# Kernel optimization log

Measured on AMD Instinct MI355X. Metric: run time of the kernel, lower is better.

Reference implementation:

```python
import jax, jax.numpy as jnp
import numpy as np

N_NODES = 100000
N_EDGES = 500000
D_IN = 128
D_HID = 256
D_OUT = 1


def mish(x):
    # x * tanh(softplus(x))
    return x * jnp.tanh(jax.nn.softplus(x))


def setup_inputs() -> dict:
    key = jax.random.key(0)
    k1, k2, k3, k4, k5, k6 = jax.random.split(key, 6)
    z = jax.random.normal(k1, (N_NODES, D_IN), dtype=jnp.float32)
    edge = jax.random.randint(k2, (2, N_EDGES), 0, N_NODES, dtype=jnp.int64)
    # PyTorch Linear default init: U(-1/sqrt(fan_in), 1/sqrt(fan_in))
    s1 = 1.0 / np.sqrt(D_IN)
    s2 = 1.0 / np.sqrt(D_HID)
    W1 = jax.random.uniform(k3, (D_HID, D_IN), minval=-s1, maxval=s1, dtype=jnp.float32)
    b1 = jax.random.uniform(k4, (D_HID,), minval=-s1, maxval=s1, dtype=jnp.float32)
    W2 = jax.random.uniform(k5, (D_OUT, D_HID), minval=-s2, maxval=s2, dtype=jnp.float32)
    b2 = jax.random.uniform(k6, (D_OUT,), minval=-s2, maxval=s2, dtype=jnp.float32)
    return {"z": z, "edge": edge, "W1": W1, "b1": b1, "W2": W2, "b2": b2}


def reference(z, edge, W1, b1, W2, b2):
    # gather node pairs and elementwise product: [E, D_IN]
    x = z[edge[0]] * z[edge[1]]
    # fc1 + mish (dropout is identity in eval mode)
    h = mish(jnp.einsum('ed,hd->eh', x, W1) + b1)
    # fc2 + sigmoid -> [E, 1]
    logits = jnp.einsum('eh,oh->eo', h, W2) + b2
    return jax.nn.sigmoid(logits)
```

## Files before the change

kernel.cpp:

```cpp
#include <hip/hip_runtime.h>
#include <hip/hip_bf16.h>
#include <hip/hip_fp16.h>
#include <type_traits>


#define N_NODES 100000
#define N_EDGES 500000
#define D_IN    128
#define D_HID   256
#define M_TILE  32
#define NTILES  (N_EDGES / M_TILE)
#define LDS_STRIDE 136
#define GRID    512
#define NWAVES  16

typedef _Float16 half8  __attribute__((ext_vector_type(8)));
typedef _Float16 half4  __attribute__((ext_vector_type(4)));
typedef __bf16   bf16x8 __attribute__((ext_vector_type(8)));
typedef float    f32x4  __attribute__((ext_vector_type(4)));
typedef float    f32x2  __attribute__((ext_vector_type(2)));

union F4H { float4 v; f32x2 h[2]; };

__device__ __forceinline__ unsigned int pkbf(f32x2 q) {
    union { __hip_bfloat162 b; unsigned int u; } c;
    c.b = __float22bfloat162_rn(make_float2(q.x, q.y));
    return c.u;
}

__device__ __forceinline__ f32x2 mish2(f32x2 x) {
    f32x2 xc = {fminf(x.x, 20.0f), fminf(x.y, 20.0f)};
    f32x2 E  = {__expf(xc.x), __expf(xc.y)};
    f32x2 num = E * (E + 2.0f);
    f32x2 den = num + 2.0f;
    f32x2 r  = {__builtin_amdgcn_rcpf(den.x), __builtin_amdgcn_rcpf(den.y)};
    return x * num * r;
}

__global__ __launch_bounds__(256)
void zcvt_kernel(const float* __restrict__ z, _Float16* __restrict__ zh) {
    const size_t i = (size_t)blockIdx.x * 256 + threadIdx.x;
    const float4 f0 = *reinterpret_cast<const float4*>(z + i * 8);
    const float4 f1 = *reinterpret_cast<const float4*>(z + i * 8 + 4);
    union { half8 h; uint4 u; } o;
    o.h[0] = (_Float16)f0.x; o.h[1] = (_Float16)f0.y;
    o.h[2] = (_Float16)f0.z; o.h[3] = (_Float16)f0.w;
    o.h[4] = (_Float16)f1.x; o.h[5] = (_Float16)f1.y;
    o.h[6] = (_Float16)f1.z; o.h[7] = (_Float16)f1.w;
    *reinterpret_cast<uint4*>(zh + i * 8) = o.u;
}

template <bool USE_H>
__global__ __launch_bounds__(1024, 8)
void edge_decoder_kernel(const float*    __restrict__ z,
                         const _Float16* __restrict__ zh,
                         const int*      __restrict__ edge,
                         const float*    __restrict__ W1,
                         const float*    __restrict__ b1,
                         const float*    __restrict__ W2,
                         const float*    __restrict__ b2,
                         float*          __restrict__ out) {
    using frag_t = std::conditional_t<USE_H, half8, bf16x8>;

    __shared__ ushort xbuf[2][M_TILE * LDS_STRIDE];
    __shared__ float  lpart[2][NWAVES][M_TILE];

    const int t    = threadIdx.x;
    const int wave = t >> 6;
    const int lane = t & 63;
    const int quad = lane >> 4;
    const int nlo  = lane & 15;

    frag_t bfrag[4];
    {
        const int n = wave * 16 + nlo;
        const float* wrow = W1 + n * D_IN;
        #pragma unroll
        for (int ks = 0; ks < 4; ++ks) {
            float4 w0 = *reinterpret_cast<const float4*>(wrow + ks * 32 + quad * 8);
            float4 w1 = *reinterpret_cast<const float4*>(wrow + ks * 32 + quad * 8 + 4);
            float wa[8] = {w0.x, w0.y, w0.z, w0.w, w1.x, w1.y, w1.z, w1.w};
            if constexpr (USE_H) {
                half8 hv;
                #pragma unroll
                for (int j = 0; j < 8; ++j) hv[j] = (_Float16)wa[j];
                bfrag[ks] = hv;
            } else {
                bf16x8 bv;
                #pragma unroll
                for (int j = 0; j < 8; ++j) bv[j] = (__bf16)wa[j];
                bfrag[ks] = bv;
            }
        }
    }
    f32x2 b1p[2], w2p[2];
    {
        const int nb = wave * 16 + quad * 4;
        b1p[0] = (f32x2){b1[nb],     b1[nb + 1]};
        b1p[1] = (f32x2){b1[nb + 2], b1[nb + 3]};
        w2p[0] = (f32x2){W2[nb],     W2[nb + 1]};
        w2p[1] = (f32x2){W2[nb + 2], W2[nb + 3]};
    }
    const float b2f = b2[0];

    const int s_slot = t >> 5;
    const int cch    = t & 31;

    int tile = blockIdx.x;
    float4 a0, c0;
    half4  ha, hc;
    {
        const int e = tile * M_TILE + s_slot;
        const int u = edge[e], v = edge[N_EDGES + e];
        if constexpr (USE_H) {
            ha = *reinterpret_cast<const half4*>(zh + (size_t)u * D_IN + cch * 4);
            hc = *reinterpret_cast<const half4*>(zh + (size_t)v * D_IN + cch * 4);
        } else {
            a0 = *reinterpret_cast<const float4*>(z + (size_t)u * D_IN + cch * 4);
            c0 = *reinterpret_cast<const float4*>(z + (size_t)v * D_IN + cch * 4);
        }
    }
    int u_n, v_n;
    {
        const int t1 = min(tile + GRID, NTILES - 1);
        const int e1 = t1 * M_TILE + s_slot;
        if constexpr (USE_H) {
            u_n = edge[e1] * 256 + cch * 8;
            v_n = edge[N_EDGES + e1] * 256 + cch * 8;
        } else {
            u_n = edge[e1]; v_n = edge[N_EDGES + e1];
        }
    }

    int  p = 0;
    bool have_prev = false;
    int  prev_base = 0;

    for (; tile < NTILES; tile += GRID) {
        if constexpr (USE_H) {
            union { half4 h; uint2 u; } pr;
            pr.h = ha * hc;
            *reinterpret_cast<uint2*>(&xbuf[p][s_slot * LDS_STRIDE + cch * 4]) = pr.u;
        } else {
            F4H A0{a0}, C0{c0};
            unsigned int r0 = pkbf(A0.h[0] * C0.h[0]);
            unsigned int r1 = pkbf(A0.h[1] * C0.h[1]);
            *reinterpret_cast<uint2*>(&xbuf[p][s_slot * LDS_STRIDE + cch * 4]) =
                make_uint2(r0, r1);
        }

        if constexpr (USE_H) {
            ha = *reinterpret_cast<const half4*>(
                     reinterpret_cast<const char*>(zh) + u_n);
            hc = *reinterpret_cast<const half4*>(
                     reinterpret_cast<const char*>(zh) + v_n);
        } else {
            a0 = *reinterpret_cast<const float4*>(z + (size_t)u_n * D_IN + cch * 4);
            c0 = *reinterpret_cast<const float4*>(z + (size_t)v_n * D_IN + cch * 4);
        }
        {
            const int t2 = min(tile + 2 * GRID, NTILES - 1);
            const int e2 = t2 * M_TILE + s_slot;
            if constexpr (USE_H) {
                u_n = edge[e2] * 256 + cch * 8;
                v_n = edge[N_EDGES + e2] * 256 + cch * 8;
            } else {
                u_n = edge[e2]; v_n = edge[N_EDGES + e2];
            }
        }

        __syncthreads();

        if (have_prev) {
            if (t < M_TILE) {
                const int pp = p ^ 1;
                float logit = b2f;
                #pragma unroll
                for (int w = 0; w < NWAVES; ++w) logit += lpart[pp][w][t];
                out[prev_base + t] = __builtin_amdgcn_rcpf(1.0f + __expf(-logit));
            }
        }

        f32x4 acc[2];
        acc[0] = (f32x4){0.f, 0.f, 0.f, 0.f};
        acc[1] = (f32x4){0.f, 0.f, 0.f, 0.f};

        #pragma unroll
        for (int ks = 0; ks < 4; ++ks) {
            frag_t af[2];
            #pragma unroll
            for (int mt = 0; mt < 2; ++mt)
                af[mt] = *reinterpret_cast<const frag_t*>(
                    &xbuf[p][(mt * 16 + nlo) * LDS_STRIDE + ks * 32 + quad * 8]);
            #pragma unroll
            for (int mt = 0; mt < 2; ++mt) {
                if constexpr (USE_H)
                    acc[mt] = __builtin_amdgcn_mfma_f32_16x16x32_f16(
                        bfrag[ks], af[mt], acc[mt], 0, 0, 0);
                else
                    acc[mt] = __builtin_amdgcn_mfma_f32_16x16x32_bf16(
                        bfrag[ks], af[mt], acc[mt], 0, 0, 0);
            }
        }

        #pragma unroll
        for (int mt = 0; mt < 2; ++mt) {
            f32x2 h0 = (f32x2){acc[mt][0], acc[mt][1]} + b1p[0];
            f32x2 h1 = (f32x2){acc[mt][2], acc[mt][3]} + b1p[1];
            f32x2 m0 = mish2(h0);
            f32x2 m1 = mish2(h1);
            f32x2 dot = m0 * w2p[0] + m1 * w2p[1];
            float s = dot.x + dot.y;
            s += __shfl_xor(s, 16);
            s += __shfl_xor(s, 32);
            if (quad == 0) lpart[p][wave][mt * 16 + nlo] = s;
        }

        have_prev = true;
        prev_base = tile * M_TILE;
        p ^= 1;
    }

    __syncthreads();
    if (have_prev && t < M_TILE) {
        const int pp = p ^ 1;
        float logit = b2f;
        #pragma unroll
        for (int w = 0; w < NWAVES; ++w) logit += lpart[pp][w][t];
        out[prev_base + t] = __builtin_amdgcn_rcpf(1.0f + __expf(-logit));
    }
}

extern "C" void kernel_launch(void* const* d_in, const int* in_sizes, int n_in,
                              void* d_out, int out_size, void* d_ws, size_t ws_size,
                              hipStream_t stream) {
    const float* z    = (const float*)d_in[0];
    const int*   edge = (const int*)d_in[1];
    const float* W1   = (const float*)d_in[2];
    const float* b1   = (const float*)d_in[3];
    const float* W2   = (const float*)d_in[4];
    const float* b2   = (const float*)d_in[5];
    float* out = (float*)d_out;

    const size_t zh_bytes = (size_t)N_NODES * D_IN * sizeof(_Float16);
    if (d_ws != nullptr && ws_size >= zh_bytes) {
        _Float16* zh = (_Float16*)d_ws;
        zcvt_kernel<<<dim3(N_NODES * D_IN / 8 / 256), dim3(256), 0, stream>>>(z, zh);
        edge_decoder_kernel<true><<<dim3(GRID), dim3(1024), 0, stream>>>(
            z, zh, edge, W1, b1, W2, b2, out);
    } else {
        edge_decoder_kernel<false><<<dim3(GRID), dim3(1024), 0, stream>>>(
            z, nullptr, edge, W1, b1, W2, b2, out);
    }
}
```

Baseline: 176.6 us.

## Stage W1 in swizzled LDS and give each wave a 32-edge tile

Restructures the edge MLP so W1 is converted to fp16/bf16 once per block into XOR-swizzled shared memory. Each wave then independently gathers 32 edges straight into MFMA operand registers and sweeps all 256 hidden units. This removes the per-tile block-wide __syncthreads, the LDS staging of gathered products and the cross-wave partial-logit reduction. In exchange, every wave re-reads all of W1 from LDS per tile, the large LDS footprint lowers occupancy, and the software prefetch of the next tile's rows is dropped.

```diff
diff --git a/kernel.cpp b/kernel.cpp
--- a/kernel.cpp
+++ b/kernel.cpp
@@ -8,33 +8,32 @@
 #define N_EDGES 500000
 #define D_IN    128
 #define D_HID   256
-#define M_TILE  32
-#define NTILES  (N_EDGES / M_TILE)
-#define LDS_STRIDE 136
+#define PAIRS   (N_EDGES / 32)
 #define GRID    512
-#define NWAVES  16
+#define TOTAL_WAVES (GRID * 16)
 
 typedef _Float16 half8  __attribute__((ext_vector_type(8)));
-typedef _Float16 half4  __attribute__((ext_vector_type(4)));
+typedef __fp16   fp16x2 __attribute__((ext_vector_type(2)));
 typedef __bf16   bf16x8 __attribute__((ext_vector_type(8)));
 typedef float    f32x4  __attribute__((ext_vector_type(4)));
-typedef float    f32x2  __attribute__((ext_vector_type(2)));
-
-union F4H { float4 v; f32x2 h[2]; };
-
-__device__ __forceinline__ unsigned int pkbf(f32x2 q) {
-    union { __hip_bfloat162 b; unsigned int u; } c;
-    c.b = __float22bfloat162_rn(make_float2(q.x, q.y));
+
+__device__ __forceinline__ unsigned int pkh_u32(float a, float b) {
+    fp16x2 r = __builtin_amdgcn_cvt_pkrtz(a, b);
+    return __builtin_bit_cast(unsigned int, r);
+}
+__device__ __forceinline__ unsigned int pkbf_u32(float a, float b) {
+    union { __hip_bfloat162 v; unsigned int u; } c;
+    c.v = __float22bfloat162_rn(make_float2(a, b));
     return c.u;
 }
 
-__device__ __forceinline__ f32x2 mish2(f32x2 x) {
-    f32x2 xc = {fminf(x.x, 20.0f), fminf(x.y, 20.0f)};
-    f32x2 E  = {__expf(xc.x), __expf(xc.y)};
-    f32x2 num = E * (E + 2.0f);
-    f32x2 den = num + 2.0f;
-    f32x2 r  = {__builtin_amdgcn_rcpf(den.x), __builtin_amdgcn_rcpf(den.y)};
-    return x * num * r;
+__device__ __forceinline__ float mishf(float x) {
+    float E   = __expf(fminf(x, 20.0f));
+    float num = E * (E + 2.0f);
+    return x * num * __builtin_amdgcn_rcpf(num + 2.0f);
+}
+__device__ __forceinline__ float sigf(float x) {
+    return __builtin_amdgcn_rcpf(1.0f + __expf(-x));
 }
 
 __global__ __launch_bounds__(256)
@@ -51,183 +50,149 @@
 }
 
 template <bool USE_H>
-__global__ __launch_bounds__(1024, 8)
-void edge_decoder_kernel(const float*    __restrict__ z,
-                         const _Float16* __restrict__ zh,
-                         const int*      __restrict__ edge,
-                         const float*    __restrict__ W1,
-                         const float*    __restrict__ b1,
-                         const float*    __restrict__ W2,
-                         const float*    __restrict__ b2,
-                         float*          __restrict__ out) {
+__global__ __launch_bounds__(1024, 4)
+void edge_mlp_kernel(const float*    __restrict__ z,
+                     const _Float16* __restrict__ zh,
+                     const int*      __restrict__ edge,
+                     const float*    __restrict__ W1,
+                     const float*    __restrict__ b1,
+                     const float*    __restrict__ W2,
+                     const float*    __restrict__ b2,
+                     float*          __restrict__ out) {
     using frag_t = std::conditional_t<USE_H, half8, bf16x8>;
 
-    __shared__ ushort xbuf[2][M_TILE * LDS_STRIDE];
-    __shared__ float  lpart[2][NWAVES][M_TILE];
-
-    const int t    = threadIdx.x;
+    __shared__ __align__(16) char smem[2048 + D_HID * D_IN * 2];
+
+    const int t = threadIdx.x;
+
+    if (t < 256) {
+        ((float*)smem)[t]          = b1[t];
+        ((float*)(smem + 1024))[t] = W2[t];
+    }
+    #pragma unroll
+    for (int i = 0; i < 4; ++i) {
+        const int c    = t + i * 1024;
+        const int h    = c >> 4;
+        const int slot = c & 15;
+        const float* src = W1 + h * D_IN + slot * 8;
+        const float4 f0 = *reinterpret_cast<const float4*>(src);
+        const float4 f1 = *reinterpret_cast<const float4*>(src + 4);
+        union { uint4 u; } o;
+        if constexpr (USE_H) {
+            o.u = make_uint4(pkh_u32(f0.x, f0.y), pkh_u32(f0.z, f0.w),
+                             pkh_u32(f1.x, f1.y), pkh_u32(f1.z, f1.w));
+        } else {
+            o.u = make_uint4(pkbf_u32(f0.x, f0.y), pkbf_u32(f0.z, f0.w),
+                             pkbf_u32(f1.x, f1.y), pkbf_u32(f1.z, f1.w));
+        }
+        char* dst = smem + 2048 + h * 256 + ((slot * 16) ^ ((h & 3) << 4));
+        *reinterpret_cast<uint4*>(dst) = o.u;
+    }
+    __syncthreads();
+
     const int wave = t >> 6;
     const int lane = t & 63;
     const int quad = lane >> 4;
     const int nlo  = lane & 15;
-
-    frag_t bfrag[4];
-    {
-        const int n = wave * 16 + nlo;
-        const float* wrow = W1 + n * D_IN;
+    const int gw   = (blockIdx.x << 4) + wave;
+
+    const char*  ldsA  = smem + 2048 + nlo * 256 + ((quad * 16) ^ ((nlo & 3) << 4));
+    const float* ldsB1 = (const float*)(smem + quad * 16);
+    const float* ldsW2 = (const float*)(smem + 1024 + quad * 16);
+    const float  b2f   = b2[0];
+
+    for (int pi = gw; pi < PAIRS; pi += TOTAL_WAVES) {
+        const int e0 = pi * 32 + nlo;
+        const int u0 = edge[e0],              v0 = edge[N_EDGES + e0];
+        const int u1 = edge[e0 + 16],         v1 = edge[N_EDGES + e0 + 16];
+
+        frag_t bf0[4], bf1[4];
+        if constexpr (USE_H) {
+            const char* zb = reinterpret_cast<const char*>(zh) + quad * 16;
+            const char* pu0 = zb + ((size_t)u0 << 8);
+            const char* pv0 = zb + ((size_t)v0 << 8);
+            const char* pu1 = zb + ((size_t)u1 << 8);
+            const char* pv1 = zb + ((size_t)v1 << 8);
+            #pragma unroll
+            for (int ks = 0; ks < 4; ++ks) {
+                half8 a = *reinterpret_cast<const half8*>(pu0 + ks * 64);
+                half8 c = *reinterpret_cast<const half8*>(pv0 + ks * 64);
+                bf0[ks] = a * c;
+            }
+            #pragma unroll
+            for (int ks = 0; ks < 4; ++ks) {
+                half8 a = *reinterpret_cast<const half8*>(pu1 + ks * 64);
+                half8 c = *reinterpret_cast<const half8*>(pv1 + ks * 64);
+                bf1[ks] = a * c;
+            }
+        } else {
+            const char* zb = reinterpret_cast<const char*>(z) + quad * 32;
+            const char* pu0 = zb + ((size_t)u0 << 9);
+            const char* pv0 = zb + ((size_t)v0 << 9);
+            const char* pu1 = zb + ((size_t)u1 << 9);
+            const char* pv1 = zb + ((size_t)v1 << 9);
+            #pragma unroll
+            for (int ks = 0; ks < 4; ++ks) {
+                float4 a0 = *reinterpret_cast<const float4*>(pu0 + ks * 128);
+                float4 a1 = *reinterpret_cast<const float4*>(pu0 + ks * 128 + 16);
+                float4 c0 = *reinterpret_cast<const float4*>(pv0 + ks * 128);
+                float4 c1 = *reinterpret_cast<const float4*>(pv0 + ks * 128 + 16);
+                union { uint4 u; bf16x8 v; } o;
+                o.u = make_uint4(pkbf_u32(a0.x*c0.x, a0.y*c0.y),
+                                 pkbf_u32(a0.z*c0.z, a0.w*c0.w),
+                                 pkbf_u32(a1.x*c1.x, a1.y*c1.y),
+                                 pkbf_u32(a1.z*c1.z, a1.w*c1.w));
+                bf0[ks] = o.v;
+            }
+            #pragma unroll
+            for (int ks = 0; ks < 4; ++ks) {
+                float4 a0 = *reinterpret_cast<const float4*>(pu1 + ks * 128);
+                float4 a1 = *reinterpret_cast<const float4*>(pu1 + ks * 128 + 16);
+                float4 c0 = *reinterpret_cast<const float4*>(pv1 + ks * 128);
+                float4 c1 = *reinterpret_cast<const float4*>(pv1 + ks * 128 + 16);
+                union { uint4 u; bf16x8 v; } o;
+                o.u = make_uint4(pkbf_u32(a0.x*c0.x, a0.y*c0.y),
+                                 pkbf_u32(a0.z*c0.z, a0.w*c0.w),
+                                 pkbf_u32(a1.x*c1.x, a1.y*c1.y),
+                                 pkbf_u32(a1.z*c1.z, a1.w*c1.w));
+                bf1[ks] = o.v;
+            }
+        }
+
+        float l0 = 0.0f, l1 = 0.0f;
         #pragma unroll
-        for (int ks = 0; ks < 4; ++ks) {
-            float4 w0 = *reinterpret_cast<const float4*>(wrow + ks * 32 + quad * 8);
-            float4 w1 = *reinterpret_cast<const float4*>(wrow + ks * 32 + quad * 8 + 4);
-            float wa[8] = {w0.x, w0.y, w0.z, w0.w, w1.x, w1.y, w1.z, w1.w};
-            if constexpr (USE_H) {
-                half8 hv;
-                #pragma unroll
-                for (int j = 0; j < 8; ++j) hv[j] = (_Float16)wa[j];
-                bfrag[ks] = hv;
-            } else {
-                bf16x8 bv;
-                #pragma unroll
-                for (int j = 0; j < 8; ++j) bv[j] = (__bf16)wa[j];
-                bfrag[ks] = bv;
-            }
-        }
-    }
-    f32x2 b1p[2], w2p[2];
-    {
-        const int nb = wave * 16 + quad * 4;
-        b1p[0] = (f32x2){b1[nb],     b1[nb + 1]};
-        b1p[1] = (f32x2){b1[nb + 2], b1[nb + 3]};
-        w2p[0] = (f32x2){W2[nb],     W2[nb + 1]};
-        w2p[1] = (f32x2){W2[nb + 2], W2[nb + 3]};
-    }
-    const float b2f = b2[0];
-
-    const int s_slot = t >> 5;
-    const int cch    = t & 31;
-
-    int tile = blockIdx.x;
-    float4 a0, c0;
-    half4  ha, hc;
-    {
-        const int e = tile * M_TILE + s_slot;
-        const int u = edge[e], v = edge[N_EDGES + e];
-        if constexpr (USE_H) {
-            ha = *reinterpret_cast<const half4*>(zh + (size_t)u * D_IN + cch * 4);
-            hc = *reinterpret_cast<const half4*>(zh + (size_t)v * D_IN + cch * 4);
-        } else {
-            a0 = *reinterpret_cast<const float4*>(z + (size_t)u * D_IN + cch * 4);
-            c0 = *reinterpret_cast<const float4*>(z + (size_t)v * D_IN + cch * 4);
-        }
-    }
-    int u_n, v_n;
-    {
-        const int t1 = min(tile + GRID, NTILES - 1);
-        const int e1 = t1 * M_TILE + s_slot;
-        if constexpr (USE_H) {
-            u_n = edge[e1] * 256 + cch * 8;
-            v_n = edge[N_EDGES + e1] * 256 + cch * 8;
-        } else {
-            u_n = edge[e1]; v_n = edge[N_EDGES + e1];
-        }
-    }
-
-    int  p = 0;
-    bool have_prev = false;
-    int  prev_base = 0;
-
-    for (; tile < NTILES; tile += GRID) {
-        if constexpr (USE_H) {
-            union { half4 h; uint2 u; } pr;
-            pr.h = ha * hc;
-            *reinterpret_cast<uint2*>(&xbuf[p][s_slot * LDS_STRIDE + cch * 4]) = pr.u;
-        } else {
-            F4H A0{a0}, C0{c0};
-            unsigned int r0 = pkbf(A0.h[0] * C0.h[0]);
-            unsigned int r1 = pkbf(A0.h[1] * C0.h[1]);
-            *reinterpret_cast<uint2*>(&xbuf[p][s_slot * LDS_STRIDE + cch * 4]) =
-                make_uint2(r0, r1);
-        }
-
-        if constexpr (USE_H) {
-            ha = *reinterpret_cast<const half4*>(
-                     reinterpret_cast<const char*>(zh) + u_n);
-            hc = *reinterpret_cast<const half4*>(
-                     reinterpret_cast<const char*>(zh) + v_n);
-        } else {
-            a0 = *reinterpret_cast<const float4*>(z + (size_t)u_n * D_IN + cch * 4);
-            c0 = *reinterpret_cast<const float4*>(z + (size_t)v_n * D_IN + cch * 4);
-        }
-        {
-            const int t2 = min(tile + 2 * GRID, NTILES - 1);
-            const int e2 = t2 * M_TILE + s_slot;
-            if constexpr (USE_H) {
-                u_n = edge[e2] * 256 + cch * 8;
-                v_n = edge[N_EDGES + e2] * 256 + cch * 8;
-            } else {
-                u_n = edge[e2]; v_n = edge[N_EDGES + e2];
-            }
-        }
-
-        __syncthreads();
-
-        if (have_prev) {
-            if (t < M_TILE) {
-                const int pp = p ^ 1;
-                float logit = b2f;
-                #pragma unroll
-                for (int w = 0; w < NWAVES; ++w) logit += lpart[pp][w][t];
-                out[prev_base + t] = __builtin_amdgcn_rcpf(1.0f + __expf(-logit));
-            }
-        }
-
-        f32x4 acc[2];
-        acc[0] = (f32x4){0.f, 0.f, 0.f, 0.f};
-        acc[1] = (f32x4){0.f, 0.f, 0.f, 0.f};
-
-        #pragma unroll
-        for (int ks = 0; ks < 4; ++ks) {
-            frag_t af[2];
-            #pragma unroll
-            for (int mt = 0; mt < 2; ++mt)
-                af[mt] = *reinterpret_cast<const frag_t*>(
-                    &xbuf[p][(mt * 16 + nlo) * LDS_STRIDE + ks * 32 + quad * 8]);
-            #pragma unroll
-            for (int mt = 0; mt < 2; ++mt) {
-                if constexpr (USE_H)
-                    acc[mt] = __builtin_amdgcn_mfma_f32_16x16x32_f16(
-                        bfrag[ks], af[mt], acc[mt], 0, 0, 0);
-                else
-                    acc[mt] = __builtin_amdgcn_mfma_f32_16x16x32_bf16(
-                        bfrag[ks], af[mt], acc[mt], 0, 0, 0);
-            }
-        }
-
-        #pragma unroll
-        for (int mt = 0; mt < 2; ++mt) {
-            f32x2 h0 = (f32x2){acc[mt][0], acc[mt][1]} + b1p[0];
-            f32x2 h1 = (f32x2){acc[mt][2], acc[mt][3]} + b1p[1];
-            f32x2 m0 = mish2(h0);
-            f32x2 m1 = mish2(h1);
-            f32x2 dot = m0 * w2p[0] + m1 * w2p[1];
-            float s = dot.x + dot.y;
-            s += __shfl_xor(s, 16);
-            s += __shfl_xor(s, 32);
-            if (quad == 0) lpart[p][wave][mt * 16 + nlo] = s;
-        }
-
-        have_prev = true;
-        prev_base = tile * M_TILE;
-        p ^= 1;
-    }
-
-    __syncthreads();
-    if (have_prev && t < M_TILE) {
-        const int pp = p ^ 1;
-        float logit = b2f;
-        #pragma unroll
-        for (int w = 0; w < NWAVES; ++w) logit += lpart[pp][w][t];
-        out[prev_base + t] = __builtin_amdgcn_rcpf(1.0f + __expf(-logit));
+        for (int g = 0; g < 16; ++g) {
+            f32x4 acc0 = (f32x4){0.f, 0.f, 0.f, 0.f};
+            f32x4 acc1 = (f32x4){0.f, 0.f, 0.f, 0.f};
+            #pragma unroll
+            for (int ks = 0; ks < 4; ++ks) {
+                frag_t wf = *reinterpret_cast<const frag_t*>(
+                                ldsA + g * 4096 + ks * 64);
+                if constexpr (USE_H) {
+                    acc0 = __builtin_amdgcn_mfma_f32_16x16x32_f16(wf, bf0[ks], acc0, 0, 0, 0);
+                    acc1 = __builtin_amdgcn_mfma_f32_16x16x32_f16(wf, bf1[ks], acc1, 0, 0, 0);
+                } else {
+                    acc0 = __builtin_amdgcn_mfma_f32_16x16x32_bf16(wf, bf0[ks], acc0, 0, 0, 0);
+                    acc1 = __builtin_amdgcn_mfma_f32_16x16x32_bf16(wf, bf1[ks], acc1, 0, 0, 0);
+                }
+            }
+            const float4 b1v = *reinterpret_cast<const float4*>(ldsB1 + g * 16);
+            const float4 w2v = *reinterpret_cast<const float4*>(ldsW2 + g * 16);
+            const float bb[4] = {b1v.x, b1v.y, b1v.z, b1v.w};
+            const float ww[4] = {w2v.x, w2v.y, w2v.z, w2v.w};
+            #pragma unroll
+            for (int i = 0; i < 4; ++i) {
+                l0 = fmaf(mishf(acc0[i] + bb[i]), ww[i], l0);
+                l1 = fmaf(mishf(acc1[i] + bb[i]), ww[i], l1);
+            }
+        }
+
+        l0 += __shfl_xor(l0, 16);  l0 += __shfl_xor(l0, 32);
+        l1 += __shfl_xor(l1, 16);  l1 += __shfl_xor(l1, 32);
+        if (quad == 0) {
+            out[pi * 32 + nlo]      = sigf(l0 + b2f);
+            out[pi * 32 + 16 + nlo] = sigf(l1 + b2f);
+        }
     }
 }
 
@@ -246,10 +211,10 @@
     if (d_ws != nullptr && ws_size >= zh_bytes) {
         _Float16* zh = (_Float16*)d_ws;
         zcvt_kernel<<<dim3(N_NODES * D_IN / 8 / 256), dim3(256), 0, stream>>>(z, zh);
-        edge_decoder_kernel<true><<<dim3(GRID), dim3(1024), 0, stream>>>(
+        edge_mlp_kernel<true><<<dim3(GRID), dim3(1024), 0, stream>>>(
             z, zh, edge, W1, b1, W2, b2, out);
     } else {
-        edge_decoder_kernel<false><<<dim3(GRID), dim3(1024), 0, stream>>>(
+        edge_mlp_kernel<false><<<dim3(GRID), dim3(1024), 0, stream>>>(
             z, nullptr, edge, W1, b1, W2, b2, out);
     }
 }
```

After: 562.0 us. 3.18x slower.
